# Performance work log

Measured on AMD Instinct MI355X. Metric: run time of the kernel, lower is better.

The kernel has to match this reference:

```python
import jax, jax.numpy as jnp
import numpy as np

B, MAX_LEN, V, H, E = 256, 31, 10000, 512, 512


def setup_inputs() -> dict:
    key = jax.random.key(0)
    ks = jax.random.split(key, 10)
    s = 0.05
    return {
        "global_images": jax.random.normal(ks[0], (B, E), jnp.float32),
        "w_input": jax.random.randint(ks[1], (B, MAX_LEN), 0, V),
        "caption_lengths": jax.random.randint(ks[2], (B,), 2, MAX_LEN + 1),
        "emb": jax.random.normal(ks[3], (V, E), jnp.float32) * s,
        "W_ih": jax.random.normal(ks[4], (4 * H, 2 * E), jnp.float32) * s,
        "W_hh": jax.random.normal(ks[5], (4 * H, H), jnp.float32) * s,
        "b_ih": jax.random.normal(ks[6], (4 * H,), jnp.float32) * s,
        "b_hh": jax.random.normal(ks[7], (4 * H,), jnp.float32) * s,
        "W_out": jax.random.normal(ks[8], (V, H), jnp.float32) * s,
        "b_out": jax.random.normal(ks[9], (V,), jnp.float32) * s,
    }


def reference(global_images, w_input, caption_lengths, emb, W_ih, W_hh, b_ih, b_hh, W_out, b_out):
    # Sort by caption length, descending (mirrors torch .sort(descending=True))
    order = jnp.argsort(-caption_lengths)
    lens = caption_lengths[order]
    w = w_input[order]                      # [B, max_len]
    g = global_images[order]                # [B, E]
    target = w[:, 1:]                       # [B, max_len-1]
    dec_len = lens - 1                      # has_end_seq_token=True

    T = w.shape[1] - 1                      # max decode steps
    h0 = jnp.zeros((g.shape[0], W_hh.shape[1]), dtype=g.dtype)
    c0 = jnp.zeros_like(h0)
    words = w[:, :T].T                      # [T, B]
    ts = jnp.arange(T)

    def step(carry, inp):
        h, c = carry
        w_t, t = inp
        x_t = jnp.concatenate([g, emb[w_t]], axis=1)          # [B, 2E]
        gates = x_t @ W_ih.T + b_ih + h @ W_hh.T + b_hh       # [B, 4H]
        i, f, gg, o = jnp.split(gates, 4, axis=1)
        i, f, o = jax.nn.sigmoid(i), jax.nn.sigmoid(f), jax.nn.sigmoid(o)
        gg = jnp.tanh(gg)
        c_new = f * c + i * gg
        h_new = o * jnp.tanh(c_new)
        active = (t < dec_len)[:, None]                       # shrinking active batch
        h = jnp.where(active, h_new, h)
        c = jnp.where(active, c_new, c)
        pt = jax.nn.log_softmax(h_new @ W_out.T + b_out, axis=1)
        pt = jnp.where(active, pt, jnp.zeros((), pt.dtype))
        return (h, c), pt

    (_, _), preds = jax.lax.scan(step, (h0, c0), (words, ts))
    preds = jnp.transpose(preds, (1, 0, 2))                   # [B, T, V]
    preds = jnp.pad(preds, ((0, 0), (0, 1), (0, 0)))          # -> [B, max_len, V]
    return preds, target, dec_len
```

## Files before the change

kernel.cpp:

```cpp
#include <hip/hip_runtime.h>
#include <hip/hip_bf16.h>
#include <math.h>

#define NB   256
#define ML   31
#define NT   30
#define NV   10000
#define NH   512
#define NE   512
#define NG   2048

#define OFF_TGT  (256LL*31LL*10000LL)
#define OFF_DEC  (OFF_TGT + 256LL*30LL)
#define PRED_B   (31LL*10000LL)

typedef __attribute__((ext_vector_type(8))) short bf16x8;
typedef __attribute__((ext_vector_type(4))) float f32x4;

__device__ inline unsigned short f2bf(float f) {
    unsigned int x = __float_as_uint(f);
    unsigned int r = x + 0x7FFFu + ((x >> 16) & 1u);
    return (unsigned short)(r >> 16);
}
__device__ inline float bf2f(unsigned short u) {
    return __uint_as_float((unsigned int)u << 16);
}

__device__ inline void gl2lds16(const void* g, void* l) {
    __builtin_amdgcn_global_load_lds(
        (const __attribute__((address_space(1))) unsigned int*)g,
        (__attribute__((address_space(3))) unsigned int*)l, 16, 0, 0);
}

__global__ void sort_k(const int* __restrict__ lens, int* __restrict__ order,
                       int* __restrict__ cnt, int* __restrict__ start,
                       int* __restrict__ flags, float* __restrict__ out_dec) {
    __shared__ int sd[NB];
    int i = threadIdx.x;
    flags[i] = 0;
    int li = lens[i];
    int r = 0;
    for (int j = 0; j < NB; j++) {
        int lj = lens[j];
        r += (lj > li) || (lj == li && j < i);
    }
    order[r] = i;
    out_dec[r] = (float)(li - 1);
    sd[r] = li - 1;
    __syncthreads();
    if (i < NT) {
        int c = 0;
        for (int b = 0; b < NB; b++) c += (sd[b] > i);
        cnt[i] = c;
    }
    __syncthreads();
    if (i == 0) {
        int s = 0;
        for (int t = 0; t < NT; t++) { start[t] = s; s += cnt[t]; }
        start[NT] = s;
    }
}

__global__ void gather_k(const float* __restrict__ gimg, const int* __restrict__ w_in,
                         const int* __restrict__ order,
                         unsigned short* __restrict__ g_sb, int* __restrict__ wsort,
                         float* __restrict__ out_tgt) {
    int r = blockIdx.x, tid = threadIdx.x;
    int o = order[r];
    for (int e = tid; e < NE; e += 256)
        g_sb[r * NE + e] = f2bf(gimg[o * NE + e]);
    if (tid < ML) wsort[r * ML + tid] = w_in[o * ML + tid];
    if (tid < NT) out_tgt[r * NT + tid] = (float)w_in[o * ML + tid + 1];
}

__global__ void rowlist_k(const int* __restrict__ wsort, const int* __restrict__ cnt,
                          const int* __restrict__ start,
                          int* __restrict__ rowlist, int* __restrict__ rowwc,
                          float* __restrict__ rowsum) {
    int t = blockIdx.x, b = threadIdx.x;
    rowsum[t * 256 + b] = 0.f;
    if (b < cnt[t]) {
        int pos = start[t] + b;
        rowlist[pos] = t * 256 + b;
        rowwc[pos] = wsort[b * ML + t];
    }
}

__global__ void prep_k(const float* __restrict__ W_ih, const float* __restrict__ W_hh,
                       const float* __restrict__ W_out, const float* __restrict__ emb,
                       unsigned short* __restrict__ Wxl, unsigned short* __restrict__ Wxb,
                       unsigned short* __restrict__ Wob, unsigned short* __restrict__ embb,
                       unsigned short* __restrict__ Wimg2) {
    int bid = blockIdx.x, tid = threadIdx.x;
    if (bid < 2048) {
        int koff = (bid < 1024) ? 0 : NE;
        unsigned short* dst = (bid < 1024) ? Wxl : Wxb;
        int gid = ((bid & 1023) << 8) + tid;
        int j = gid >> 7, k4 = gid & 127;
        float4 v = *(const float4*)(W_ih + (size_t)j * (2 * NE) + koff + k4 * 4);
        ushort4 o;
        o.x = f2bf(v.x); o.y = f2bf(v.y); o.z = f2bf(v.z); o.w = f2bf(v.w);
        *(ushort4*)(dst + (size_t)j * NE + k4 * 4) = o;
    } else if (bid < 12048) {
        const float* src = (bid < 7048) ? W_out : emb;
        unsigned short* dst = (bid < 7048) ? Wob : embb;
        int gid = ((bid < 7048 ? bid - 2048 : bid - 7048) << 8) + tid;
        float4 v = ((const float4*)src)[gid];
        ushort4 o;
        o.x = f2bf(v.x); o.y = f2bf(v.y); o.z = f2bf(v.z); o.w = f2bf(v.w);
        ((ushort4*)dst)[gid] = o;
    } else {
        int gid = ((bid - 12048) << 8) + tid;
        int hi = gid & 3, kt = (gid >> 2) & 15, R = (gid >> 6) & 127, s = gid >> 13;
        int q = R >> 5, ct = (R >> 4) & 1, lo = R & 15;
        int col = q * 512 + s * 32 + ct * 16 + lo;
        int k = kt * 32 + hi * 8;
        const float* src = W_hh + (size_t)col * NH + k;
        __align__(16) unsigned short o[8];
#pragma unroll
        for (int j = 0; j < 8; ++j) o[j] = f2bf(src[j]);
        int ba = (R << 10) + ((kt * 64 + hi * 16) ^ ((lo & 7) << 4));
        *(uint4*)((char*)Wimg2 + ((size_t)s << 17) + ba) = *(const uint4*)o;
    }
}

__launch_bounds__(256)
__global__ void gxgemm(const unsigned short* __restrict__ Abf,
                       const unsigned short* __restrict__ Bbf,
                       const float* __restrict__ bias1, const float* __restrict__ bias2,
                       float* __restrict__ outf) {
    __shared__ __align__(16) char Bs[131072];
    int m0 = blockIdx.y * 128, n0 = blockIdx.x * 128;
    int tid = threadIdx.x;
    int lane = tid & 63, w = tid >> 6;
    int wy = w >> 1, wx = w & 1;

#pragma unroll 4
    for (int p = 0; p < 32; ++p) {
        int row = (tid >> 6) + (p << 2);
        uint4 v = *(const uint4*)(Bbf + ((size_t)(n0 + row) << 9) + ((tid & 63) << 3));
        int ba = (row << 10) + ((tid & 63) << 4); ba ^= (row & 7) << 4;
        *(uint4*)(Bs + ba) = v;
    }
    const unsigned short* aptr[4];
#pragma unroll
    for (int rt = 0; rt < 4; ++rt)
        aptr[rt] = Abf + ((size_t)(m0 + (wy << 6) + (rt << 4) + (lane & 15)) << 9);

    f32x4 acc[4][4];
#pragma unroll
    for (int i = 0; i < 4; ++i)
#pragma unroll
        for (int j = 0; j < 4; ++j) acc[i][j] = (f32x4){0.f, 0.f, 0.f, 0.f};
    __syncthreads();

#pragma unroll 4
    for (int ks = 0; ks < 16; ++ks) {
        int koff = (ks << 5) + ((lane >> 4) << 3);
        bf16x8 bq[4];
#pragma unroll
        for (int ct = 0; ct < 4; ++ct) {
            int brow = (wx << 6) + (ct << 4) + (lane & 15);
            int bb = (brow << 10) + (koff << 1); bb ^= (brow & 7) << 4;
            bq[ct] = *(const bf16x8*)(Bs + bb);
        }
#pragma unroll
        for (int rt = 0; rt < 4; ++rt) {
            bf16x8 aq = *(const bf16x8*)(aptr[rt] + koff);
#pragma unroll
            for (int ct = 0; ct < 4; ++ct)
                acc[rt][ct] = __builtin_amdgcn_mfma_f32_16x16x32_bf16(aq, bq[ct], acc[rt][ct], 0, 0, 0);
        }
    }
#pragma unroll
    for (int rt = 0; rt < 4; ++rt)
#pragma unroll
        for (int ct = 0; ct < 4; ++ct) {
            int n = n0 + (wx << 6) + (ct << 4) + (lane & 15);
            float badd = bias1[n] + bias2[n];
#pragma unroll
            for (int ri = 0; ri < 4; ++ri) {
                int m = m0 + (wy << 6) + (rt << 4) + ((lane >> 4) << 2) + ri;
                outf[(size_t)m * NG + n] = acc[rt][ct][ri] + badd;
            }
        }
}

template <int AMODE, int EPI>
__launch_bounds__(256)
__global__ void pgemm(const unsigned short* __restrict__ Abf,
                      const int* __restrict__ ridx,
                      const unsigned short* __restrict__ Aemb,
                      const unsigned short* __restrict__ Bbf,
                      int N,
                      const int* __restrict__ mact_p,
                      const float* __restrict__ bias1,
                      const int* __restrict__ rowlist,
                      float* __restrict__ outf,
                      unsigned short* __restrict__ outb,
                      float* __restrict__ rowsum) {
    __shared__ __align__(16) char lds[65536];
    int Mact = *mact_p;
    int m0 = blockIdx.y * 128;
    if (m0 >= Mact) return;
    int n0 = blockIdx.x * 128;
    int tid = threadIdx.x;
    int lane = tid & 63, w = tid >> 6;
    int wy = w >> 1, wx = w & 1;
    int hi = lane >> 4, lo = lane & 15;

    const char* asrc[4];
#pragma unroll
    for (int i = 0; i < 4; ++i) {
        int p = (i << 8) + tid;
        int ma = m0 + (p >> 3); if (ma > Mact - 1) ma = Mact - 1;
        if (AMODE == 0) asrc[i] = (const char*)Abf + ((size_t)ma << 10);
        else            asrc[i] = (const char*)Aemb + ((size_t)ridx[ma] << 10);
    }

    auto stage = [&](int kt, int buf) {
#pragma unroll
        for (int i = 0; i < 4; ++i) {
            int p = (i << 8) + tid;
            int row = p >> 3, sc = (p & 7) ^ (row & 7);
            gl2lds16(asrc[i] + (kt << 7) + (sc << 4), lds + (buf << 14) + (p << 4));
        }
#pragma unroll
        for (int i = 0; i < 4; ++i) {
            int p = (i << 8) + tid;
            int row = p >> 3, sc = (p & 7) ^ (row & 7);
            int nb = n0 + row; if (nb > N - 1) nb = N - 1;
            gl2lds16((const char*)Bbf + ((size_t)nb << 10) + (kt << 7) + (sc << 4),
                     lds + 32768 + (buf << 14) + (p << 4));
        }
    };

    f32x4 acc[4][4];
#pragma unroll
    for (int i = 0; i < 4; ++i)
#pragma unroll
        for (int j = 0; j < 4; ++j) acc[i][j] = (f32x4){0.f, 0.f, 0.f, 0.f};

    stage(0, 0);
    __syncthreads();

    for (int kt = 0; kt < 8; ++kt) {
        int buf = kt & 1;
        if (kt < 7) stage(kt + 1, buf ^ 1);
#pragma unroll
        for (int kc = 0; kc < 2; ++kc) {
            bf16x8 aq[4], bq[4];
#pragma unroll
            for (int rt = 0; rt < 4; ++rt) {
                int ra = (wy << 6) + (rt << 4) + lo;
                int cha = ((kc << 2) + hi) ^ (ra & 7);
                aq[rt] = *(const bf16x8*)(lds + (buf << 14) + (ra << 7) + (cha << 4));
                int cb = (wx << 6) + (rt << 4) + lo;
                int chb = ((kc << 2) + hi) ^ (cb & 7);
                bq[rt] = *(const bf16x8*)(lds + 32768 + (buf << 14) + (cb << 7) + (chb << 4));
            }
#pragma unroll
            for (int rt = 0; rt < 4; ++rt)
#pragma unroll
                for (int ct = 0; ct < 4; ++ct)
                    acc[rt][ct] = __builtin_amdgcn_mfma_f32_16x16x32_bf16(aq[rt], bq[ct], acc[rt][ct], 0, 0, 0);
        }
        __syncthreads();
    }

    if (EPI == 0) {
#pragma unroll
        for (int rt = 0; rt < 4; ++rt)
#pragma unroll
            for (int ct = 0; ct < 4; ++ct) {
                int n = n0 + (wx << 6) + (ct << 4) + lo;
#pragma unroll
                for (int ri = 0; ri < 4; ++ri) {
                    int m = m0 + (wy << 6) + (rt << 4) + (hi << 2) + ri;
                    if (m < Mact) {
                        int b = rowlist[m] & 255;
                        float v = acc[rt][ct][ri] + bias1[(size_t)b * NG + n];
                        outb[(size_t)m * NG + ((n & 511) << 2) + (n >> 9)] = f2bf(v);
                    }
                }
            }
    } else {
#pragma unroll
        for (int rt = 0; rt < 4; ++rt) {
            float es4[4] = {0.f, 0.f, 0.f, 0.f};
#pragma unroll
            for (int ct = 0; ct < 4; ++ct) {
                int n = n0 + (wx << 6) + (ct << 4) + lo;
                bool okn = (n < N);
                float bo = okn ? bias1[n] : 0.f;
#pragma unroll
                for (int ri = 0; ri < 4; ++ri) {
                    int m = m0 + (wy << 6) + (rt << 4) + (hi << 2) + ri;
                    float v = acc[rt][ct][ri] + bo;
                    if (okn && m < Mact) {
                        int r = rowlist[m];
                        outf[(size_t)(r & 255) * PRED_B + (size_t)(r >> 8) * NV + n] = v;
                        es4[ri] += __expf(v);
                    }
                }
            }
#pragma unroll
            for (int ri = 0; ri < 4; ++ri) {
                float s = es4[ri];
                s += __shfl_xor(s, 1); s += __shfl_xor(s, 2);
                s += __shfl_xor(s, 4); s += __shfl_xor(s, 8);
                if (lo == 0) {
                    int m = m0 + (wy << 6) + (rt << 4) + (hi << 2) + ri;
                    if (m < Mact) atomicAdd(&rowsum[m], s);
                }
            }
        }
    }
}

__launch_bounds__(256, 1)
__global__ void lstmy_k(const unsigned short* __restrict__ Wimg2,
                        const unsigned short* __restrict__ gallc,
                        unsigned short* __restrict__ hx,
                        unsigned short* __restrict__ h_allc,
                        int* __restrict__ flags,
                        const int* __restrict__ cnt,
                        const int* __restrict__ start) {
    __shared__ __align__(16) char Wlds[131072];
    __shared__ __align__(16) char hlds[16384];
    __shared__ float Gs[4 * 16 * 32];
    __shared__ __align__(16) unsigned short hstg[16 * 32];
    int tid = threadIdx.x;
    int g = blockIdx.x & 15, s = blockIdx.x >> 4;
    int lane = tid & 63, w = tid >> 6;
    int hi = lane >> 4, lo = lane & 15;
    int q = w;

    {
        const char* wsrc = (const char*)Wimg2 + ((size_t)s << 17) + tid * 16;
#pragma unroll 8
        for (int r = 0; r < 32; ++r)
            gl2lds16(wsrc + r * 4096, Wlds + tid * 16 + r * 4096);
    }
    {
        uint4 z = make_uint4(0u, 0u, 0u, 0u);
        *(uint4*)(hlds + tid * 16) = z;
        *(uint4*)(hlds + 4096 + tid * 16) = z;
        *(uint4*)(hlds + 8192 + tid * 16) = z;
        *(uint4*)(hlds + 12288 + tid * 16) = z;
    }
    asm volatile("s_waitcnt vmcnt(0)" ::: "memory");
    __syncthreads();

    int row = tid >> 4, d0 = tid & 15;
    float creg[2] = {0.f, 0.f};

    for (int t = 0; t < NT; ++t) {
        int cnt_t = cnt[t];
        if (16 * g >= cnt_t) break;
        int nrow = cnt_t - 16 * g; if (nrow > 16) nrow = 16;
        int pos0 = start[t] + 16 * g;

        int rr = row < nrow ? row : nrow - 1;
        const unsigned short* gp = gallc + ((size_t)(pos0 + rr) << 11);
        uint2 gq0 = *(const uint2*)(gp + (s * 32 + d0) * 4);
        uint2 gq1 = *(const uint2*)(gp + (s * 32 + d0 + 16) * 4);

        if (t > 0) {
            if (tid < 16) {
                const int* fp = flags + g * 16 + tid;
                int f;
                do {
                    asm volatile("global_load_dword %0, %1, off sc0 sc1\n\t"
                                 "s_waitcnt vmcnt(0)"
                                 : "=v"(f) : "v"(fp) : "memory");
                } while (f < t);
            }
            __syncthreads();
            const char* hsrc = (const char*)hx +
                ((size_t)(((t - 1) & 1) * 16 + g) << 14) + tid * 16;
            uint4 va, vb, vc, vd;
            asm volatile(
                "global_load_dwordx4 %0, %4, off sc0 sc1\n\t"
                "global_load_dwordx4 %1, %5, off sc0 sc1\n\t"
                "global_load_dwordx4 %2, %6, off sc0 sc1\n\t"
                "global_load_dwordx4 %3, %7, off sc0 sc1\n\t"
                "s_waitcnt vmcnt(0)"
                : "=&v"(va), "=&v"(vb), "=&v"(vc), "=&v"(vd)
                : "v"(hsrc), "v"(hsrc + 4096), "v"(hsrc + 8192), "v"(hsrc + 12288)
                : "memory");
            *(uint4*)(hlds + tid * 16) = va;
            *(uint4*)(hlds + 4096 + tid * 16) = vb;
            *(uint4*)(hlds + 8192 + tid * 16) = vc;
            *(uint4*)(hlds + 12288 + tid * 16) = vd;
            __syncthreads();
        }

        f32x4 acc[2];
        acc[0] = (f32x4){0.f, 0.f, 0.f, 0.f};
        acc[1] = (f32x4){0.f, 0.f, 0.f, 0.f};
#pragma unroll 4
        for (int kt = 0; kt < 16; ++kt) {
            int ab = (lo << 10) + (((kt << 5) + (hi << 3)) << 1); ab ^= (lo & 7) << 4;
            bf16x8 aq = *(const bf16x8*)(hlds + ab);
#pragma unroll
            for (int ct = 0; ct < 2; ++ct) {
                int R = (q * 2 + ct) * 16 + lo;
                int bb = (R << 10) + ((kt * 64 + hi * 16) ^ ((lo & 7) << 4));
                bf16x8 bq = *(const bf16x8*)(Wlds + bb);
                acc[ct] = __builtin_amdgcn_mfma_f32_16x16x32_bf16(aq, bq, acc[ct], 0, 0, 0);
            }
        }
#pragma unroll
        for (int ct = 0; ct < 2; ++ct)
#pragma unroll
            for (int ri = 0; ri < 4; ++ri)
                Gs[(q * 16 + hi * 4 + ri) * 32 + ct * 16 + lo] = acc[ct][ri];
        __syncthreads();

        bool act = row < nrow;
#pragma unroll
        for (int p = 0; p < 2; ++p) {
            int dp = d0 + p * 16;
            int hd = s * 32 + dp;
            const unsigned short* gq = (const unsigned short*)(p ? &gq1 : &gq0);
            float iv = Gs[(0 * 16 + row) * 32 + dp] + bf2f(gq[0]);
            float fv = Gs[(1 * 16 + row) * 32 + dp] + bf2f(gq[1]);
            float gv = Gs[(2 * 16 + row) * 32 + dp] + bf2f(gq[2]);
            float ov = Gs[(3 * 16 + row) * 32 + dp] + bf2f(gq[3]);
            float i_ = 1.f / (1.f + __expf(-iv));
            float f_ = 1.f / (1.f + __expf(-fv));
            float o_ = 1.f / (1.f + __expf(-ov));
            float ea = __expf(-2.f * fabsf(gv));
            float th = (1.f - ea) / (1.f + ea);
            th = (gv < 0.f) ? -th : th;
            float cn = f_ * creg[p] + i_ * th;
            float ec = __expf(-2.f * fabsf(cn));
            float tc = (1.f - ec) / (1.f + ec);
            tc = (cn < 0.f) ? -tc : tc;
            float hn = o_ * tc;
            unsigned short hv;
            if (act) {
                creg[p] = cn;
                hv = f2bf(hn);
            } else {
                int hoff = ((row << 10) + (hd << 1)) ^ ((row & 7) << 4);
                hv = *(const unsigned short*)(hlds + hoff);
            }
            hstg[row * 32 + dp] = hv;
        }
        __syncthreads();

        uint2 v0, v1;
        int crow = tid >> 2, j = tid & 3;
        if (tid < 64) {
            v0 = *(const uint2*)(hstg + crow * 32 + j * 8);
            v1 = *(const uint2*)(hstg + crow * 32 + j * 8 + 4);
            char* himg = (char*)hx + ((size_t)((t & 1) * 16 + g) << 14);
            int dstoff = (crow << 10) + ((((s << 2) + j) ^ (crow & 7)) << 4);
            asm volatile("global_store_dwordx2 %0, %2, off sc0 sc1\n\t"
                         "global_store_dwordx2 %1, %3, off sc0 sc1"
                         :: "v"(himg + dstoff), "v"(himg + dstoff + 8),
                            "v"(v0), "v"(v1) : "memory");
        }
        asm volatile("s_waitcnt vmcnt(0)" ::: "memory");
        __syncthreads();
        if (tid == 0) {
            int fv = t + 1;
            asm volatile("global_store_dword %0, %1, off sc0 sc1"
                         :: "v"(flags + g * 16 + s), "v"(fv) : "memory");
        }
        if (tid < 64 && crow < nrow) {
            unsigned short* hap = h_allc + (size_t)(pos0 + crow) * NH + s * 32 + j * 8;
            *(uint2*)hap = v0;
            *(uint2*)(hap + 4) = v1;
        }
    }
}

__global__ void norm_k(float* __restrict__ out, const float* __restrict__ rowsum,
                       const int* __restrict__ cnt, const int* __restrict__ start) {
    int r = blockIdx.x;
    int t = r >> 8, b = r & 255;
    bool act = (t < NT) && (b < cnt[t]);
    float lse = 0.f;
    if (act) lse = logf(rowsum[start[t] + b]);
    float4* row = (float4*)(out + (size_t)b * PRED_B + (size_t)t * NV);
    for (int v4 = threadIdx.x; v4 < NV / 4; v4 += 256) {
        float4 x;
        if (act) {
            x = row[v4];
            x.x -= lse; x.y -= lse; x.z -= lse; x.w -= lse;
        } else {
            x.x = 0.f; x.y = 0.f; x.z = 0.f; x.w = 0.f;
        }
        row[v4] = x;
    }
}

extern "C" void kernel_launch(void* const* d_in, const int* in_sizes, int n_in,
                              void* d_out, int out_size, void* d_ws, size_t ws_size,
                              hipStream_t stream) {
    const float* gimg  = (const float*)d_in[0];
    const int*   w_in  = (const int*)d_in[1];
    const int*   lens  = (const int*)d_in[2];
    const float* emb   = (const float*)d_in[3];
    const float* W_ih  = (const float*)d_in[4];
    const float* W_hh  = (const float*)d_in[5];
    const float* b_ih  = (const float*)d_in[6];
    const float* b_hh  = (const float*)d_in[7];
    const float* W_out = (const float*)d_in[8];
    const float* b_out = (const float*)d_in[9];
    float* out = (float*)d_out;

    char* p = (char*)d_ws;
    auto alloc = [&](size_t bytes) -> char* {
        char* r = p;
        p += (bytes + 255) & ~(size_t)255;
        return r;
    };
    int*   order   = (int*)alloc(NB * 4);
    int*   wsort   = (int*)alloc(NB * ML * 4);
    int*   cnt     = (int*)alloc(NT * 4);
    int*   start   = (int*)alloc((NT + 1) * 4);
    int*   flags   = (int*)alloc(256 * 4);
    int*   rowlist = (int*)alloc((size_t)NT * NB * 4);
    int*   rowwc   = (int*)alloc((size_t)NT * NB * 4);
    float* gx      = (float*)alloc((size_t)NB * NG * 4);
    float* rowsum  = (float*)alloc((size_t)NT * NB * 4);
    unsigned short* g_sb   = (unsigned short*)alloc((size_t)NB * NE * 2);
    unsigned short* hx     = (unsigned short*)alloc((size_t)2 * 16 * 16384);
    unsigned short* h_allc = (unsigned short*)alloc((size_t)NT * NB * NH * 2);
    unsigned short* Wimg2  = (unsigned short*)alloc((size_t)NG * NH * 2);
    unsigned short* Wxl    = (unsigned short*)alloc((size_t)NG * NE * 2);
    unsigned short* Wxb    = (unsigned short*)alloc((size_t)NG * NE * 2);
    unsigned short* Wob    = (unsigned short*)alloc((size_t)NV * NH * 2);
    unsigned short* embb   = (unsigned short*)alloc((size_t)NV * NE * 2);
    unsigned short* gallc  = (unsigned short*)alloc((size_t)NT * NB * NG * 2);
    int* nact = start + NT;

    sort_k<<<1, 256, 0, stream>>>(lens, order, cnt, start, flags, out + OFF_DEC);
    gather_k<<<NB, 256, 0, stream>>>(gimg, w_in, order, g_sb, wsort, out + OFF_TGT);
    rowlist_k<<<NT, 256, 0, stream>>>(wsort, cnt, start, rowlist, rowwc, rowsum);
    prep_k<<<12560, 256, 0, stream>>>(W_ih, W_hh, W_out, emb, Wxl, Wxb, Wob, embb, Wimg2);

    gxgemm<<<dim3(NG / 128, NB / 128), 256, 0, stream>>>(g_sb, Wxl, b_ih, b_hh, gx);

    pgemm<1, 0><<<dim3(NG / 128, NT * NB / 128), 256, 0, stream>>>(
        nullptr, rowwc, embb, Wxb, NG, nact, gx, rowlist, nullptr, gallc, nullptr);

    {
        void* cargs[] = { (void*)&Wimg2, (void*)&gallc, (void*)&hx, (void*)&h_allc,
                          (void*)&flags, (void*)&cnt, (void*)&start };
        (void)hipLaunchCooperativeKernel((void*)lstmy_k, dim3(256), dim3(256), cargs, 0, stream);
    }

    pgemm<0, 1><<<dim3((NV + 127) / 128, NT * NB / 128), 256, 0, stream>>>(
        h_allc, nullptr, nullptr, Wob, NV, nact, b_out, rowlist, out, nullptr, rowsum);

    norm_k<<<(NT + 1) * NB, 256, 0, stream>>>(out, rowsum, cnt, start);
}
```

Measured before the change: 435.0 us.

## Stage logits in bf16 scratch, swap GEMM grid order, load h into registers

```diff
diff --git a/kernel.cpp b/kernel.cpp
--- a/kernel.cpp
+++ b/kernel.cpp
@@ -196,14 +196,13 @@
                       const int* __restrict__ mact_p,
                       const float* __restrict__ bias1,
                       const int* __restrict__ rowlist,
-                      float* __restrict__ outf,
                       unsigned short* __restrict__ outb,
                       float* __restrict__ rowsum) {
     __shared__ __align__(16) char lds[65536];
     int Mact = *mact_p;
-    int m0 = blockIdx.y * 128;
+    int m0 = blockIdx.x * 128;
     if (m0 >= Mact) return;
-    int n0 = blockIdx.x * 128;
+    int n0 = blockIdx.y * 128;
     int tid = threadIdx.x;
     int lane = tid & 63, w = tid >> 6;
     int wy = w >> 1, wx = w & 1;
@@ -298,8 +297,7 @@
                     int m = m0 + (wy << 6) + (rt << 4) + (hi << 2) + ri;
                     float v = acc[rt][ct][ri] + bo;
                     if (okn && m < Mact) {
-                        int r = rowlist[m];
-                        outf[(size_t)(r & 255) * PRED_B + (size_t)(r >> 8) * NV + n] = v;
+                        outb[(size_t)m * NV + n] = f2bf(v);
                         es4[ri] += __expf(v);
                     }
                 }
@@ -327,7 +325,6 @@
                         const int* __restrict__ cnt,
                         const int* __restrict__ start) {
     __shared__ __align__(16) char Wlds[131072];
-    __shared__ __align__(16) char hlds[16384];
     __shared__ float Gs[4 * 16 * 32];
     __shared__ __align__(16) unsigned short hstg[16 * 32];
     int tid = threadIdx.x;
@@ -342,13 +339,6 @@
         for (int r = 0; r < 32; ++r)
             gl2lds16(wsrc + r * 4096, Wlds + tid * 16 + r * 4096);
     }
-    {
-        uint4 z = make_uint4(0u, 0u, 0u, 0u);
-        *(uint4*)(hlds + tid * 16) = z;
-        *(uint4*)(hlds + 4096 + tid * 16) = z;
-        *(uint4*)(hlds + 8192 + tid * 16) = z;
-        *(uint4*)(hlds + 12288 + tid * 16) = z;
-    }
     asm volatile("s_waitcnt vmcnt(0)" ::: "memory");
     __syncthreads();
 
@@ -366,49 +356,39 @@
         uint2 gq0 = *(const uint2*)(gp + (s * 32 + d0) * 4);
         uint2 gq1 = *(const uint2*)(gp + (s * 32 + d0 + 16) * 4);
 
+        f32x4 acc[2];
+        acc[0] = (f32x4){0.f, 0.f, 0.f, 0.f};
+        acc[1] = (f32x4){0.f, 0.f, 0.f, 0.f};
+
         if (t > 0) {
-            if (tid < 16) {
-                const int* fp = flags + g * 16 + tid;
+            {
+                const int* fp = flags + g * 16 + lo;
                 int f;
                 do {
                     asm volatile("global_load_dword %0, %1, off sc0 sc1\n\t"
                                  "s_waitcnt vmcnt(0)"
                                  : "=v"(f) : "v"(fp) : "memory");
-                } while (f < t);
-            }
-            __syncthreads();
-            const char* hsrc = (const char*)hx +
-                ((size_t)(((t - 1) & 1) * 16 + g) << 14) + tid * 16;
-            uint4 va, vb, vc, vd;
-            asm volatile(
-                "global_load_dwordx4 %0, %4, off sc0 sc1\n\t"
-                "global_load_dwordx4 %1, %5, off sc0 sc1\n\t"
-                "global_load_dwordx4 %2, %6, off sc0 sc1\n\t"
-                "global_load_dwordx4 %3, %7, off sc0 sc1\n\t"
-                "s_waitcnt vmcnt(0)"
-                : "=&v"(va), "=&v"(vb), "=&v"(vc), "=&v"(vd)
-                : "v"(hsrc), "v"(hsrc + 4096), "v"(hsrc + 8192), "v"(hsrc + 12288)
-                : "memory");
-            *(uint4*)(hlds + tid * 16) = va;
-            *(uint4*)(hlds + 4096 + tid * 16) = vb;
-            *(uint4*)(hlds + 8192 + tid * 16) = vc;
-            *(uint4*)(hlds + 12288 + tid * 16) = vd;
-            __syncthreads();
-        }
-
-        f32x4 acc[2];
-        acc[0] = (f32x4){0.f, 0.f, 0.f, 0.f};
-        acc[1] = (f32x4){0.f, 0.f, 0.f, 0.f};
-#pragma unroll 4
-        for (int kt = 0; kt < 16; ++kt) {
-            int ab = (lo << 10) + (((kt << 5) + (hi << 3)) << 1); ab ^= (lo & 7) << 4;
-            bf16x8 aq = *(const bf16x8*)(hlds + ab);
-#pragma unroll
-            for (int ct = 0; ct < 2; ++ct) {
-                int R = (q * 2 + ct) * 16 + lo;
-                int bb = (R << 10) + ((kt * 64 + hi * 16) ^ ((lo & 7) << 4));
-                bf16x8 bq = *(const bf16x8*)(Wlds + bb);
-                acc[ct] = __builtin_amdgcn_mfma_f32_16x16x32_bf16(aq, bq, acc[ct], 0, 0, 0);
+                } while (__any(f < t));
+            }
+            const char* hb = (const char*)hx +
+                ((size_t)(((t - 1) & 1) * 16 + g) << 14) + (lo << 6) + (hi << 4);
+            uint4 hv[16];
+#pragma unroll
+            for (int c = 0; c < 16; ++c)
+                asm volatile("global_load_dwordx4 %0, %1, off sc0 sc1"
+                             : "=v"(hv[c]) : "v"(hb + (c << 10)) : "memory");
+            asm volatile("s_waitcnt vmcnt(0)" ::: "memory");
+            __builtin_amdgcn_sched_barrier(0);
+#pragma unroll
+            for (int kt = 0; kt < 16; ++kt) {
+                bf16x8 aq = *(const bf16x8*)&hv[kt];
+#pragma unroll
+                for (int ct = 0; ct < 2; ++ct) {
+                    int R = (q * 2 + ct) * 16 + lo;
+                    int bb = (R << 10) + ((kt * 64 + hi * 16) ^ ((lo & 7) << 4));
+                    bf16x8 bq = *(const bf16x8*)(Wlds + bb);
+                    acc[ct] = __builtin_amdgcn_mfma_f32_16x16x32_bf16(aq, bq, acc[ct], 0, 0, 0);
+                }
             }
         }
 #pragma unroll
@@ -422,7 +402,6 @@
 #pragma unroll
         for (int p = 0; p < 2; ++p) {
             int dp = d0 + p * 16;
-            int hd = s * 32 + dp;
             const unsigned short* gq = (const unsigned short*)(p ? &gq1 : &gq0);
             float iv = Gs[(0 * 16 + row) * 32 + dp] + bf2f(gq[0]);
             float fv = Gs[(1 * 16 + row) * 32 + dp] + bf2f(gq[1]);
@@ -439,15 +418,14 @@
             float tc = (1.f - ec) / (1.f + ec);
             tc = (cn < 0.f) ? -tc : tc;
             float hn = o_ * tc;
-            unsigned short hv;
+            unsigned short hv16;
             if (act) {
                 creg[p] = cn;
-                hv = f2bf(hn);
+                hv16 = f2bf(hn);
             } else {
-                int hoff = ((row << 10) + (hd << 1)) ^ ((row & 7) << 4);
-                hv = *(const unsigned short*)(hlds + hoff);
-            }
-            hstg[row * 32 + dp] = hv;
+                hv16 = hstg[row * 32 + dp];
+            }
+            hstg[row * 32 + dp] = hv16;
         }
         __syncthreads();
 
@@ -457,7 +435,7 @@
             v0 = *(const uint2*)(hstg + crow * 32 + j * 8);
             v1 = *(const uint2*)(hstg + crow * 32 + j * 8 + 4);
             char* himg = (char*)hx + ((size_t)((t & 1) * 16 + g) << 14);
-            int dstoff = (crow << 10) + ((((s << 2) + j) ^ (crow & 7)) << 4);
+            int dstoff = (s << 10) + (crow << 6) + (j << 4);
             asm volatile("global_store_dwordx2 %0, %2, off sc0 sc1\n\t"
                          "global_store_dwordx2 %1, %3, off sc0 sc1"
                          :: "v"(himg + dstoff), "v"(himg + dstoff + 8),
@@ -478,23 +456,35 @@
     }
 }
 
-__global__ void norm_k(float* __restrict__ out, const float* __restrict__ rowsum,
+__global__ void norm_k(float* __restrict__ out, const unsigned short* __restrict__ logitb,
+                       const float* __restrict__ rowsum,
                        const int* __restrict__ cnt, const int* __restrict__ start) {
     int r = blockIdx.x;
     int t = r >> 8, b = r & 255;
     bool act = (t < NT) && (b < cnt[t]);
-    float lse = 0.f;
-    if (act) lse = logf(rowsum[start[t] + b]);
     float4* row = (float4*)(out + (size_t)b * PRED_B + (size_t)t * NV);
-    for (int v4 = threadIdx.x; v4 < NV / 4; v4 += 256) {
-        float4 x;
-        if (act) {
-            x = row[v4];
-            x.x -= lse; x.y -= lse; x.z -= lse; x.w -= lse;
-        } else {
-            x.x = 0.f; x.y = 0.f; x.z = 0.f; x.w = 0.f;
-        }
-        row[v4] = x;
+    int tid = threadIdx.x;
+    if (act) {
+        int pos = start[t] + b;
+        float lse = logf(rowsum[pos]);
+        const uint4* lrow = (const uint4*)(logitb + (size_t)pos * NV);
+        for (int v8 = tid; v8 < NV / 8; v8 += 256) {
+            uint4 u = lrow[v8];
+            float4 a, c;
+            a.x = bf2f((unsigned short)u.x) - lse;
+            a.y = bf2f((unsigned short)(u.x >> 16)) - lse;
+            a.z = bf2f((unsigned short)u.y) - lse;
+            a.w = bf2f((unsigned short)(u.y >> 16)) - lse;
+            c.x = bf2f((unsigned short)u.z) - lse;
+            c.y = bf2f((unsigned short)(u.z >> 16)) - lse;
+            c.z = bf2f((unsigned short)u.w) - lse;
+            c.w = bf2f((unsigned short)(u.w >> 16)) - lse;
+            row[v8 * 2] = a;
+            row[v8 * 2 + 1] = c;
+        }
+    } else {
+        float4 z = make_float4(0.f, 0.f, 0.f, 0.f);
+        for (int v4 = tid; v4 < NV / 4; v4 += 256) row[v4] = z;
     }
 }
 
@@ -537,6 +527,7 @@
     unsigned short* Wob    = (unsigned short*)alloc((size_t)NV * NH * 2);
     unsigned short* embb   = (unsigned short*)alloc((size_t)NV * NE * 2);
     unsigned short* gallc  = (unsigned short*)alloc((size_t)NT * NB * NG * 2);
+    unsigned short* logitb = (unsigned short*)alloc((size_t)NT * NB * NV * 2);
     int* nact = start + NT;
 
     sort_k<<<1, 256, 0, stream>>>(lens, order, cnt, start, flags, out + OFF_DEC);
@@ -546,8 +537,8 @@
 
     gxgemm<<<dim3(NG / 128, NB / 128), 256, 0, stream>>>(g_sb, Wxl, b_ih, b_hh, gx);
 
-    pgemm<1, 0><<<dim3(NG / 128, NT * NB / 128), 256, 0, stream>>>(
-        nullptr, rowwc, embb, Wxb, NG, nact, gx, rowlist, nullptr, gallc, nullptr);
+    pgemm<1, 0><<<dim3(NT * NB / 128, NG / 128), 256, 0, stream>>>(
+        nullptr, rowwc, embb, Wxb, NG, nact, gx, rowlist, gallc, nullptr);
 
     {
         void* cargs[] = { (void*)&Wimg2, (void*)&gallc, (void*)&hx, (void*)&h_allc,
@@ -555,8 +546,8 @@
         (void)hipLaunchCooperativeKernel((void*)lstmy_k, dim3(256), dim3(256), cargs, 0, stream);
     }
 
-    pgemm<0, 1><<<dim3((NV + 127) / 128, NT * NB / 128), 256, 0, stream>>>(
-        h_allc, nullptr, nullptr, Wob, NV, nact, b_out, rowlist, out, nullptr, rowsum);
-
-    norm_k<<<(NT + 1) * NB, 256, 0, stream>>>(out, rowsum, cnt, start);
-}
+    pgemm<0, 1><<<dim3(NT * NB / 128, (NV + 127) / 128), 256, 0, stream>>>(
+        h_allc, nullptr, nullptr, Wob, NV, nact, b_out, rowlist, logitb, rowsum);
+
+    norm_k<<<(NT + 1) * NB, 256, 0, stream>>>(out, logitb, rowsum, cnt, start);
+}
```

Result: faster. 423.9 us (-2.5%).
